# Kernel tuning notes

Measured on AMD Instinct MI355X. Metric: run time of the kernel, lower is better.

The kernel has to match this reference:

```python
import jax, jax.numpy as jnp
import numpy as np

B, S, D_MODEL = 2, 2048, 2048
N_HEADS, N_KV_HEADS, D_HEAD = 32, 8, 64
INIT_STD = 0.02


def setup_inputs() -> dict:
    key = jax.random.key(0)
    k1, k2, k3, k4, k5 = jax.random.split(key, 5)
    return {
        "residual": jax.random.normal(k1, (B, S, D_MODEL), dtype=jnp.float32),
        "W_Q": jax.random.normal(k2, (N_HEADS, D_HEAD, D_MODEL), dtype=jnp.float32) * INIT_STD,
        "W_K": jax.random.normal(k3, (N_KV_HEADS, D_HEAD, D_MODEL), dtype=jnp.float32) * INIT_STD,
        "W_V": jax.random.normal(k4, (N_KV_HEADS, D_HEAD, D_MODEL), dtype=jnp.float32) * INIT_STD,
        "W_O": jax.random.normal(k5, (N_HEADS, D_HEAD, D_MODEL), dtype=jnp.float32) * INIT_STD,
    }


def reference(residual, W_Q, W_K, W_V, W_O):
    # QKV projections: residual [b,p,d] x W [n,h,d] -> [b,p,n,h]
    q = jnp.einsum('bpd,nhd->bpnh', residual, W_Q)
    k = jnp.einsum('bpd,nhd->bpnh', residual, W_K)
    v = jnp.einsum('bpd,nhd->bpnh', residual, W_V)

    # GQA: repeat_interleave kv heads up to n_heads
    rep = N_HEADS // N_KV_HEADS
    k = jnp.repeat(k, rep, axis=2)  # [b, p, n_heads, h]
    v = jnp.repeat(v, rep, axis=2)

    # scaled dot-product scores: [b, n, q, k]
    scores = jnp.einsum('bqnh,bknh->bnqk', q, k) / jnp.sqrt(jnp.float32(D_HEAD))

    # causal mask (seq_len == total_len, no cache)
    seq_len = residual.shape[1]
    causal = jnp.tril(jnp.ones((seq_len, seq_len), dtype=bool))
    scores = jnp.where(causal[None, None, :, :], scores, jnp.float32(-jnp.inf))

    pattern = jax.nn.softmax(scores, axis=-1)

    # weighted sum of values: [b, q, n, h]
    attn_out = jnp.einsum('bnqk,bknh->bqnh', pattern, v)

    # output projection: [b, q, d_model]
    out = jnp.einsum('bqnh,nhd->bqd', attn_out, W_O)
    return out
```

## Files before the change

### kernel.cpp

```cpp
#include <hip/hip_runtime.h>


typedef __attribute__((ext_vector_type(8))) short short8;
typedef __attribute__((ext_vector_type(4))) short short4v;
typedef __attribute__((ext_vector_type(4))) float f32x4;

__device__ __forceinline__ short f2bs(float f) {
  unsigned u = __float_as_uint(f);
  u = (u + 0x7fffu + ((u >> 16) & 1u)) >> 16;
  return (short)u;
}
__device__ __forceinline__ float bs2f(short s) {
  return __uint_as_float(((unsigned)(unsigned short)s) << 16);
}

__device__ __forceinline__ void async_ld16(const void* g, void* l) {
  __builtin_amdgcn_global_load_lds((__attribute__((address_space(1))) void*)(g),
                                   (__attribute__((address_space(3))) void*)(l),
                                   16, 0, 0);
}

#define BARRIER()                       \
  do {                                  \
    asm volatile("" ::: "memory");      \
    __builtin_amdgcn_s_barrier();       \
    asm volatile("" ::: "memory");      \
  } while (0)
#define LGKM0()                                          \
  do {                                                   \
    asm volatile("s_waitcnt lgkmcnt(0)" ::: "memory");   \
    __builtin_amdgcn_sched_barrier(0);                   \
  } while (0)
#define VMCNT(n) asm volatile("s_waitcnt vmcnt(" #n ")" ::: "memory")
#define MFMA16(a, b, c) \
  (c) = __builtin_amdgcn_mfma_f32_16x16x32_bf16((a), (b), (c), 0, 0, 0)

__device__ __forceinline__ short4v pk4bf16(float p0, float p1, float p2,
                                           float p3) {
  union {
    unsigned u[2];
    short4v s;
  } pk;
  asm("v_cvt_pk_bf16_f32 %0, %1, %2" : "=v"(pk.u[0]) : "v"(p0), "v"(p1));
  asm("v_cvt_pk_bf16_f32 %0, %1, %2" : "=v"(pk.u[1]) : "v"(p2), "v"(p3));
  return pk.s;
}

__device__ __forceinline__ int block_sniff_f32(const short* __restrict__ r,
                                               int* bad) {
  if (threadIdx.x == 0) *bad = 0;
  __syncthreads();
  int my = 0;
  for (int i = threadIdx.x; i < 512; i += blockDim.x) {
    float x = bs2f(r[i]);
    if (!(fabsf(x) < 100.0f)) my = 1;
  }
  if (my) atomicOr(bad, 1);
  __syncthreads();
  return *bad;
}

__global__ __launch_bounds__(256) void prep_kernel(
    const void* __restrict__ s0, const void* __restrict__ s1,
    const void* __restrict__ s2, const void* __restrict__ s3,
    short* __restrict__ d0, short* __restrict__ d1, short* __restrict__ d2,
    short* __restrict__ d3, const void* __restrict__ wo,
    short* __restrict__ wot) {
  __shared__ short tile[64][65];
  __shared__ int badsh;
  const int isf = block_sniff_f32((const short*)s0, &badsh);
  const int bid = blockIdx.x;
  if (bid < 7168) {
    long off = (long)bid * 256 + threadIdx.x;
    const void* src;
    short* dst;
    if (off < 1048576) {
      src = s0; dst = d0;
    } else if ((off -= 1048576) < 524288) {
      src = s1; dst = d1;
    } else if ((off -= 524288) < 131072) {
      src = s2; dst = d2;
    } else {
      off -= 131072; src = s3; dst = d3;
    }
    const long e = off * 8;
    short8 v;
    if (isf) {
      const float* f = (const float*)src + e;
      const f32x4 a = *(const f32x4*)(f);
      const f32x4 b = *(const f32x4*)(f + 4);
#pragma unroll
      for (int j = 0; j < 4; ++j) {
        v[j] = f2bs(a[j]);
        v[4 + j] = f2bs(b[j]);
      }
    } else {
      v = *(const short8*)((const short*)src + e);
    }
    *(short8*)(dst + e) = v;
  } else {
    const int tb = bid - 7168;
    const int bx = tb & 31, by = tb >> 5;
    const int tx = threadIdx.x & 63, ty = threadIdx.x >> 6;
#pragma unroll
    for (int i = 0; i < 16; ++i) {
      const int r = ty + i * 4;
      const size_t idx = (size_t)(by * 64 + r) * 2048 + bx * 64 + tx;
      tile[r][tx] =
          isf ? f2bs(((const float*)wo)[idx]) : ((const short*)wo)[idx];
    }
    __syncthreads();
#pragma unroll
    for (int i = 0; i < 16; ++i) {
      const int r = ty + i * 4;
      wot[(size_t)(bx * 64 + r) * 2048 + by * 64 + tx] = tile[tx][r];
    }
  }
}

__device__ __forceinline__ void gemm256(const short* __restrict__ A, int lda,
                                        const short* __restrict__ B, int ldb,
                                        void* __restrict__ C, int ldc,
                                        int rowBase, int colBase, int K,
                                        short* SM, int outF32, int outT,
                                        float cscale) {
  const int t = threadIdx.x;
  const int wave = t >> 6;
  const int lane = t & 63;
  const int quad = lane >> 4;
  const int m16 = lane & 15;
  const int wr = (wave >> 2) * 128;
  const int wc = (wave & 3) * 64;

  short* const As0 = SM;
  short* const As1 = SM + 16384;
  short* const Bs0 = SM + 32768;
  short* const Bs1 = SM + 49152;

  const int sr = t >> 3;
  const int sc8 = ((t & 7) ^ (sr & 7)) * 8;
  const short* aS = A + (size_t)(rowBase + sr) * lda + sc8;
  const short* bS = B + (size_t)(colBase + sr) * ldb + sc8;
  const int dOff = wave * 512;

#define STG_A(buf, rg, kt) \
  async_ld16(aS + (size_t)(rg) * lda + (kt) * 64, (buf) + (rg) * 64 + dOff)
#define STG_B(buf, rg, kt) \
  async_ld16(bS + (size_t)(rg) * ldb + (kt) * 64, (buf) + (rg) * 64 + dOff)
#define RD(buf, row0, kh)                          \
  (*(const short8*)((buf) + ((row0) + m16) * 64 +  \
                    ((((kh) * 4 + quad) ^ (m16 & 7)) * 8)))

  const int nT = K >> 6;
  STG_A(As0, 0, 0); STG_A(As0, 64, 0); STG_A(As0, 128, 0); STG_A(As0, 192, 0);
  STG_B(Bs0, 0, 0); STG_B(Bs0, 64, 0); STG_B(Bs0, 128, 0); STG_B(Bs0, 192, 0);
  if (nT > 1) {
    STG_A(As1, 0, 1); STG_A(As1, 64, 1); STG_A(As1, 128, 1); STG_A(As1, 192, 1);
  }

  f32x4 acc[8][4] = {};
  for (int tt = 0; tt < nT; ++tt) {
    short* const Ac = (tt & 1) ? As1 : As0;
    short* const Bc = (tt & 1) ? Bs1 : Bs0;
    short* const Bn = (tt & 1) ? Bs0 : Bs1;

    if (tt + 1 < nT) {
      VMCNT(4);
    } else {
      VMCNT(0);
    }
    BARRIER();

    if (tt + 1 < nT) {
      STG_B(Bn, 0, tt + 1); STG_B(Bn, 64, tt + 1);
      STG_B(Bn, 128, tt + 1); STG_B(Bn, 192, tt + 1);
    }

    short8 alo[4][2], blo[2][2], bhi[2][2];
#pragma unroll
    for (int i = 0; i < 4; ++i) {
      alo[i][0] = RD(Ac, wr + i * 16, 0);
      alo[i][1] = RD(Ac, wr + i * 16, 1);
    }
#pragma unroll
    for (int j = 0; j < 2; ++j) {
      blo[j][0] = RD(Bc, wc + j * 16, 0);
      blo[j][1] = RD(Bc, wc + j * 16, 1);
    }
#pragma unroll
    for (int i = 0; i < 4; ++i)
#pragma unroll
      for (int j = 0; j < 2; ++j) {
        MFMA16(alo[i][0], blo[j][0], acc[i][j]);
        MFMA16(alo[i][1], blo[j][1], acc[i][j]);
      }
#pragma unroll
    for (int j = 0; j < 2; ++j) {
      bhi[j][0] = RD(Bc, wc + 32 + j * 16, 0);
      bhi[j][1] = RD(Bc, wc + 32 + j * 16, 1);
    }
#pragma unroll
    for (int i = 0; i < 4; ++i)
#pragma unroll
      for (int j = 0; j < 2; ++j) {
        MFMA16(alo[i][0], bhi[j][0], acc[i][2 + j]);
        MFMA16(alo[i][1], bhi[j][1], acc[i][2 + j]);
      }

    short8 ahi[4][2];
#pragma unroll
    for (int i = 0; i < 4; ++i) {
      ahi[i][0] = RD(Ac, wr + 64 + i * 16, 0);
      ahi[i][1] = RD(Ac, wr + 64 + i * 16, 1);
    }
    LGKM0();
    BARRIER();

    if (tt + 2 < nT) {
      STG_A(Ac, 0, tt + 2); STG_A(Ac, 64, tt + 2);
      STG_A(Ac, 128, tt + 2); STG_A(Ac, 192, tt + 2);
    }

#pragma unroll
    for (int i = 0; i < 4; ++i)
#pragma unroll
      for (int j = 0; j < 2; ++j) {
        MFMA16(ahi[i][0], blo[j][0], acc[4 + i][j]);
        MFMA16(ahi[i][1], blo[j][1], acc[4 + i][j]);
      }
#pragma unroll
    for (int i = 0; i < 4; ++i)
#pragma unroll
      for (int j = 0; j < 2; ++j) {
        MFMA16(ahi[i][0], bhi[j][0], acc[4 + i][2 + j]);
        MFMA16(ahi[i][1], bhi[j][1], acc[4 + i][2 + j]);
      }
  }

  float* const F = (float*)SM + wave * 4096;
#pragma unroll
  for (int h = 0; h < 2; ++h) {
    if (h) LGKM0();
#pragma unroll
    for (int i = 0; i < 4; ++i)
#pragma unroll
      for (int j = 0; j < 4; ++j)
#pragma unroll
        for (int r = 0; r < 4; ++r)
          F[(i * 16 + quad * 4 + r) * 64 + j * 16 + m16] =
              acc[h * 4 + i][j][r] * cscale;
    LGKM0();
    if (outT) {
      const int bb = rowBase >> 11;
      const int pBase = (rowBase & 2047) + wr + h * 64;
#pragma unroll
      for (int p2 = 0; p2 < 16; ++p2) {
        const int hl = p2 * 4 + quad;
        short4v s;
#pragma unroll
        for (int r = 0; r < 4; ++r) s[r] = f2bs(F[(m16 * 4 + r) * 64 + hl]);
        *(short4v*)((short*)C +
                    ((size_t)(bb * 512 + colBase + wc + hl)) * ldc + pBase +
                    m16 * 4) = s;
      }
    } else {
#pragma unroll
      for (int p = 0; p < 16; ++p) {
        const int row = p * 4 + quad;
        const f32x4 vv = *(const f32x4*)(F + row * 64 + m16 * 4);
        const size_t gi = (size_t)(rowBase + wr + h * 64 + row) * ldc +
                          colBase + wc + m16 * 4;
        if (outF32) {
          *(f32x4*)((float*)C + gi) = vv;
        } else {
          short4v s;
#pragma unroll
          for (int r = 0; r < 4; ++r) s[r] = f2bs(vv[r]);
          *(short4v*)((short*)C + gi) = s;
        }
      }
    }
  }
#undef STG_A
#undef STG_B
#undef RD
}

__device__ __forceinline__ void gemm256x128(const short* __restrict__ A,
                                            int lda,
                                            const short* __restrict__ B,
                                            int ldb, void* __restrict__ C,
                                            int ldc, int rowBase, int colBase,
                                            int K, short* SM, int outF32) {
  const int t = threadIdx.x;
  const int wave = t >> 6;
  const int lane = t & 63;
  const int quad = lane >> 4;
  const int m16 = lane & 15;
  const int wr = (wave >> 1) * 64;
  const int wc = (wave & 1) * 64;

  short* const As0 = SM;
  short* const As1 = SM + 16384;
  short* const Bs0 = SM + 32768;
  short* const Bs1 = SM + 40960;

  const int sr = t >> 3;
  const int sc8 = ((t & 7) ^ (sr & 7)) * 8;
  const short* aS = A + (size_t)(rowBase + sr) * lda + sc8;
  const short* bS = B + (size_t)(colBase + sr) * ldb + sc8;
  const int dOff = wave * 512;

#define STG_A(buf, rg, kt) \
  async_ld16(aS + (size_t)(rg) * lda + (kt) * 64, (buf) + (rg) * 64 + dOff)
#define STG_B(buf, rg, kt) \
  async_ld16(bS + (size_t)(rg) * ldb + (kt) * 64, (buf) + (rg) * 64 + dOff)
#define RD(buf, row0, kh)                          \
  (*(const short8*)((buf) + ((row0) + m16) * 64 +  \
                    ((((kh) * 4 + quad) ^ (m16 & 7)) * 8)))

  const int nT = K >> 6;
  STG_A(As0, 0, 0); STG_A(As0, 64, 0); STG_A(As0, 128, 0); STG_A(As0, 192, 0);
  STG_B(Bs0, 0, 0); STG_B(Bs0, 64, 0);
  if (nT > 1) {
    STG_A(As1, 0, 1); STG_A(As1, 64, 1); STG_A(As1, 128, 1); STG_A(As1, 192, 1);
  }

  f32x4 acc[4][4] = {};
  for (int tt = 0; tt < nT; ++tt) {
    short* const Ac = (tt & 1) ? As1 : As0;
    short* const Bc = (tt & 1) ? Bs1 : Bs0;
    short* const Bn = (tt & 1) ? Bs0 : Bs1;

    if (tt + 1 < nT) {
      VMCNT(4);
    } else {
      VMCNT(0);
    }
    BARRIER();

    if (tt + 1 < nT) { STG_B(Bn, 0, tt + 1); STG_B(Bn, 64, tt + 1); }

    short8 a0[4], b0[4];
#pragma unroll
    for (int i = 0; i < 4; ++i) a0[i] = RD(Ac, wr + i * 16, 0);
#pragma unroll
    for (int j = 0; j < 4; ++j) b0[j] = RD(Bc, wc + j * 16, 0);
#pragma unroll
    for (int i = 0; i < 4; ++i)
#pragma unroll
      for (int j = 0; j < 4; ++j) MFMA16(a0[i], b0[j], acc[i][j]);

    short8 a1[4], b1[4];
#pragma unroll
    for (int i = 0; i < 4; ++i) a1[i] = RD(Ac, wr + i * 16, 1);
#pragma unroll
    for (int j = 0; j < 4; ++j) b1[j] = RD(Bc, wc + j * 16, 1);
    LGKM0();
    BARRIER();

    if (tt + 2 < nT) {
      STG_A(Ac, 0, tt + 2); STG_A(Ac, 64, tt + 2);
      STG_A(Ac, 128, tt + 2); STG_A(Ac, 192, tt + 2);
    }

#pragma unroll
    for (int i = 0; i < 4; ++i)
#pragma unroll
      for (int j = 0; j < 4; ++j) MFMA16(a1[i], b1[j], acc[i][j]);
  }

  float* const F = (float*)SM + wave * 4096;
#pragma unroll
  for (int i = 0; i < 4; ++i)
#pragma unroll
    for (int j = 0; j < 4; ++j)
#pragma unroll
      for (int r = 0; r < 4; ++r)
        F[(i * 16 + quad * 4 + r) * 64 + j * 16 + m16] = acc[i][j][r];
  LGKM0();
#pragma unroll
  for (int p = 0; p < 16; ++p) {
    const int row = p * 4 + quad;
    const f32x4 vv = *(const f32x4*)(F + row * 64 + m16 * 4);
    const size_t gi =
        (size_t)(rowBase + wr + row) * ldc + colBase + wc + m16 * 4;
    if (outF32) {
      *(f32x4*)((float*)C + gi) = vv;
    } else {
      short4v s;
#pragma unroll
      for (int r = 0; r < 4; ++r) s[r] = f2bs(vv[r]);
      *(short4v*)((short*)C + gi) = s;
    }
  }
#undef STG_A
#undef STG_B
#undef RD
}

__global__ __launch_bounds__(512, 2) void qkv_gemm_kernel(
    const short* __restrict__ R, const short* __restrict__ WQ,
    const short* __restrict__ WK, const short* __restrict__ WV,
    short* __restrict__ q, short* __restrict__ k, short* __restrict__ vtb) {
  __shared__ __align__(16) short SM[65536];
  const int lid = blockIdx.x;
  const int nl = (lid & 7) * 24 + (lid >> 3);
  const int ct = nl % 12;
  const int rt = nl / 12;
  const short* Bm;
  short* Cout;
  int colBase, ldc, outT = 0;
  float cs = 1.0f;
  if (ct < 8) {
    Bm = WQ; Cout = q; colBase = ct * 256; ldc = 2048;
    cs = 0.125f * 1.44269504088896340736f;
  } else if (ct < 10) {
    Bm = WK; Cout = k; colBase = (ct - 8) * 256; ldc = 512;
  } else {
    Bm = WV; Cout = vtb; colBase = (ct - 10) * 256; ldc = 2048; outT = 1;
  }
  gemm256(R, 2048, Bm, 2048, Cout, ldc, rt * 256, colBase, 2048, SM, 0, outT,
          cs);
}

__global__ __launch_bounds__(512, 2) void out_gemm_kernel(
    const short* __restrict__ A, const short* __restrict__ Bt,
    void* __restrict__ C, const short* __restrict__ sniffsrc) {
  __shared__ __align__(16) short SM[65536];
  const int outF32 = block_sniff_f32(sniffsrc, (int*)SM);
  const int lid = blockIdx.x;
  const int nl = (lid & 7) * 32 + (lid >> 3);
  const int ct = nl & 15;
  const int rt = nl >> 4;
  gemm256x128(A, 2048, Bt, 2048, C, 2048, rt * 256, ct * 128, 2048, SM,
              outF32);
}

__global__ __launch_bounds__(256, 3) void attn_kernel(
    const short* __restrict__ qbuf, const short* __restrict__ kbuf,
    const short* __restrict__ vtb, short* __restrict__ obuf) {
  __shared__ __align__(16) short Ks[2][64 * 64];
  __shared__ __align__(16) short Vs[2][64 * 64];
  __shared__ __align__(16) short Pb[4][32 * 64];

  const int b = blockIdx.x >> 3;
  const int kv = blockIdx.x & 7;
  const int qc = 63 - blockIdx.y;
  const int t = threadIdx.x;
  const int wave = t >> 6;
  const int hd = kv * 4 + wave;
  const int lane = t & 63;
  const int quad = lane >> 4;
  const int col = lane & 15;
  const int rb0 = qc * 32;

  short8 qf[2][2];
#pragma unroll
  for (int nt = 0; nt < 2; ++nt) {
    const int qr = rb0 + nt * 16 + col;
    const short* qp = qbuf + ((size_t)(b * 2048 + qr)) * 2048 + hd * 64 + quad * 8;
    qf[nt][0] = *(const short8*)(qp);
    qf[nt][1] = *(const short8*)(qp + 32);
  }

  short8 ones;
#pragma unroll
  for (int i = 0; i < 8; ++i) ones[i] = (short)0x3F80;

  f32x4 oacc[2][4] = {};
  f32x4 sacc[2] = {};

  short* P = &Pb[wave][0];
  const int swz = 4 * (col & 3);

  const int sRow = t >> 3;
  const int sPos = t & 7;
  const int r1 = sRow + 32;
  const short* kRow0 = kbuf + ((size_t)(b * 2048 + sRow)) * 512 + kv * 64 +
                       ((sPos ^ (sRow & 7)) * 8);
  const short* kRow1 = kbuf + ((size_t)(b * 2048 + r1)) * 512 + kv * 64 +
                       ((sPos ^ (r1 & 7)) * 8);
  const short* vRow0 = vtb + ((size_t)(b * 512 + kv * 64 + sRow)) * 2048 +
                       ((sPos ^ (sRow & 7)) * 8);
  const short* vRow1 = vtb + ((size_t)(b * 512 + kv * 64 + r1)) * 2048 +
                       ((sPos ^ (r1 & 7)) * 8);

  const int nkt = (qc >> 1) + 1;

  async_ld16(kRow0, &Ks[0][wave * 512]);
  async_ld16(kRow1, &Ks[0][2048 + wave * 512]);
  async_ld16(vRow0, &Vs[0][wave * 512]);
  async_ld16(vRow1, &Vs[0][2048 + wave * 512]);

  for (int kt = 0; kt < nkt; ++kt) {
    __syncthreads();
    if (kt + 1 < nkt) {
      const int nb = (kt + 1) & 1;
      const size_t ko = (size_t)(kt + 1) * 64 * 512;
      const int vo = (kt + 1) * 64;
      async_ld16(kRow0 + ko, &Ks[nb][wave * 512]);
      async_ld16(kRow1 + ko, &Ks[nb][2048 + wave * 512]);
      async_ld16(vRow0 + vo, &Vs[nb][wave * 512]);
      async_ld16(vRow1 + vo, &Vs[nb][2048 + wave * 512]);
    }
    const int ktb = kt * 64;
    const short* ks = &Ks[kt & 1][0];
    const short* vs = &Vs[kt & 1][0];

    short8 kf[4][2];
#pragma unroll
    for (int mt = 0; mt < 4; ++mt) {
      const int krow = mt * 16 + col;
      kf[mt][0] = *(const short8*)(ks + krow * 64 + ((quad ^ (col & 7)) * 8));
      kf[mt][1] = *(const short8*)(ks + krow * 64 + (((4 + quad) ^ (col & 7)) * 8));
    }

#pragma unroll
    for (int nt = 0; nt < 2; ++nt) {
      const int rb = rb0 + nt * 16;

      f32x4 st[4];
      __builtin_amdgcn_s_setprio(1);
#pragma unroll
      for (int mt = 0; mt < 4; ++mt) {
        f32x4 z = {0.f, 0.f, 0.f, 0.f};
        z = __builtin_amdgcn_mfma_f32_16x16x32_bf16(kf[mt][0], qf[nt][0], z, 0, 0, 0);
        z = __builtin_amdgcn_mfma_f32_16x16x32_bf16(kf[mt][1], qf[nt][1], z, 0, 0, 0);
        st[mt] = z;
      }
      __builtin_amdgcn_s_setprio(0);

      if (ktb + 63 > rb) {
        const int qrow = rb + col;
#pragma unroll
        for (int mt = 0; mt < 4; ++mt)
#pragma unroll
          for (int r = 0; r < 4; ++r)
            if (ktb + mt * 16 + quad * 4 + r > qrow) st[mt][r] = -1.0e30f;
      }

#pragma unroll
      for (int mt = 0; mt < 4; ++mt) {
        const float p0 = exp2f(st[mt][0]);
        const float p1 = exp2f(st[mt][1]);
        const float p2 = exp2f(st[mt][2]);
        const float p3 = exp2f(st[mt][3]);
        *(short4v*)(P + (nt * 16 + col) * 64 + (quad + 4 * (mt ^ (col & 3))) * 4) =
            pk4bf16(p0, p1, p2, p3);
      }
    }

    asm volatile("s_waitcnt lgkmcnt(0)" ::: "memory");

    short8 pf[2][2];
#pragma unroll
    for (int nt = 0; nt < 2; ++nt) {
      const int base = (nt * 16 + col) * 64;
      pf[nt][0] = *(const short8*)(P + base + ((2 * quad) ^ swz) * 4);
      pf[nt][1] = *(const short8*)(P + base + ((8 + 2 * quad) ^ swz) * 4);
    }

    __builtin_amdgcn_s_setprio(1);
#pragma unroll
    for (int nt = 0; nt < 2; ++nt) {
      sacc[nt] = __builtin_amdgcn_mfma_f32_16x16x32_bf16(ones, pf[nt][0],
                                                         sacc[nt], 0, 0, 0);
      sacc[nt] = __builtin_amdgcn_mfma_f32_16x16x32_bf16(ones, pf[nt][1],
                                                         sacc[nt], 0, 0, 0);
    }

#pragma unroll
    for (int ct = 0; ct < 4; ++ct) {
      const int h = ct * 16 + col;
      const short8 va = *(const short8*)(vs + h * 64 + ((quad ^ (col & 7)) * 8));
      const short8 vb = *(const short8*)(vs + h * 64 + (((4 + quad) ^ (col & 7)) * 8));
#pragma unroll
      for (int nt = 0; nt < 2; ++nt) {
        oacc[nt][ct] = __builtin_amdgcn_mfma_f32_16x16x32_bf16(
            va, pf[nt][0], oacc[nt][ct], 0, 0, 0);
        oacc[nt][ct] = __builtin_amdgcn_mfma_f32_16x16x32_bf16(
            vb, pf[nt][1], oacc[nt][ct], 0, 0, 0);
      }
    }
    __builtin_amdgcn_s_setprio(0);
  }

  const float inv0 = 1.0f / sacc[0][0];
  const float inv1 = 1.0f / sacc[1][0];
#pragma unroll
  for (int nt = 0; nt < 2; ++nt) {
    const float inv = nt ? inv1 : inv0;
#pragma unroll
    for (int ct = 0; ct < 4; ++ct) {
      *(short4v*)(P + (nt * 16 + col) * 64 + ct * 16 + quad * 4) =
          pk4bf16(oacc[nt][ct][0] * inv, oacc[nt][ct][1] * inv,
                  oacc[nt][ct][2] * inv, oacc[nt][ct][3] * inv);
    }
  }
  asm volatile("s_waitcnt lgkmcnt(0)" ::: "memory");
#pragma unroll
  for (int p = 0; p < 4; ++p) {
    const int qlocal = (lane >> 3) + 8 * p;
    const short8 row = *(const short8*)(P + qlocal * 64 + (lane & 7) * 8);
    *(short8*)(obuf + ((size_t)(b * 2048 + rb0 + qlocal)) * 2048 + hd * 64 +
               (lane & 7) * 8) = row;
  }
}

extern "C" void kernel_launch(void* const* d_in, const int* in_sizes, int n_in,
                              void* d_out, int out_size, void* d_ws,
                              size_t ws_size, hipStream_t stream) {
  char* ws = (char*)d_ws;
  short* rbuf = (short*)(ws + 256);
  short* wqb = rbuf + 8388608;
  short* wkb = wqb + 4194304;
  short* wvb = wkb + 1048576;
  short* kbuf = wvb + 1048576;
  short* vtb = kbuf + 2097152;
  short* abuf = vtb + 2097152;
  short* wot = abuf + 8388608;
  short* qbuf = (short*)d_out;

  hipLaunchKernelGGL(prep_kernel, dim3(8192), dim3(256), 0, stream,
                     d_in[0], d_in[1], d_in[2], d_in[3], rbuf, wqb, wkb, wvb,
                     d_in[4], wot);
  hipLaunchKernelGGL(qkv_gemm_kernel, dim3(192), dim3(512), 0, stream,
                     rbuf, wqb, wkb, wvb, qbuf, kbuf, vtb);
  hipLaunchKernelGGL(attn_kernel, dim3(16, 64), dim3(256), 0, stream,
                     qbuf, kbuf, vtb, abuf);
  hipLaunchKernelGGL(out_gemm_kernel, dim3(256), dim3(512), 0, stream,
                     abuf, wot, (void*)d_out, (const short*)d_in[0]);
}
```

Before: 289.9 us.

## Switch QKV GEMM to 256x128 tiles, double-buffer B, drop attention setprio

Removes the 256x256 GEMM path and runs the QKV projection on the 256x128 tile routine, extended with output scaling and a transposed-output mode. This doubles the grid from 192 to 384 blocks to fill more CUs. The 256x128 routine now prefetches B two tiles ahead, like A, instead of one. The s_setprio hints around the MFMA blocks in the attention kernel are removed. The smaller tiles mean more operand traffic per FLOP.

```diff
diff --git a/kernel.cpp b/kernel.cpp
--- a/kernel.cpp
+++ b/kernel.cpp
@@ -118,24 +118,25 @@
   }
 }
 
-__device__ __forceinline__ void gemm256(const short* __restrict__ A, int lda,
-                                        const short* __restrict__ B, int ldb,
-                                        void* __restrict__ C, int ldc,
-                                        int rowBase, int colBase, int K,
-                                        short* SM, int outF32, int outT,
-                                        float cscale) {
+__device__ __forceinline__ void gemm256x128(const short* __restrict__ A,
+                                            int lda,
+                                            const short* __restrict__ B,
+                                            int ldb, void* __restrict__ C,
+                                            int ldc, int rowBase, int colBase,
+                                            int K, short* SM, int outF32,
+                                            int outT, float cscale) {
   const int t = threadIdx.x;
   const int wave = t >> 6;
   const int lane = t & 63;
   const int quad = lane >> 4;
   const int m16 = lane & 15;
-  const int wr = (wave >> 2) * 128;
-  const int wc = (wave & 3) * 64;
+  const int wr = (wave >> 1) * 64;
+  const int wc = (wave & 1) * 64;
 
   short* const As0 = SM;
   short* const As1 = SM + 16384;
   short* const Bs0 = SM + 32768;
-  short* const Bs1 = SM + 49152;
+  short* const Bs1 = SM + 40960;
 
   const int sr = t >> 3;
   const int sc8 = ((t & 7) ^ (sr & 7)) * 8;
@@ -153,193 +154,23 @@
 
   const int nT = K >> 6;
   STG_A(As0, 0, 0); STG_A(As0, 64, 0); STG_A(As0, 128, 0); STG_A(As0, 192, 0);
-  STG_B(Bs0, 0, 0); STG_B(Bs0, 64, 0); STG_B(Bs0, 128, 0); STG_B(Bs0, 192, 0);
-  if (nT > 1) {
-    STG_A(As1, 0, 1); STG_A(As1, 64, 1); STG_A(As1, 128, 1); STG_A(As1, 192, 1);
-  }
-
-  f32x4 acc[8][4] = {};
-  for (int tt = 0; tt < nT; ++tt) {
-    short* const Ac = (tt & 1) ? As1 : As0;
-    short* const Bc = (tt & 1) ? Bs1 : Bs0;
-    short* const Bn = (tt & 1) ? Bs0 : Bs1;
-
-    if (tt + 1 < nT) {
-      VMCNT(4);
-    } else {
-      VMCNT(0);
-    }
-    BARRIER();
-
-    if (tt + 1 < nT) {
-      STG_B(Bn, 0, tt + 1); STG_B(Bn, 64, tt + 1);
-      STG_B(Bn, 128, tt + 1); STG_B(Bn, 192, tt + 1);
-    }
-
-    short8 alo[4][2], blo[2][2], bhi[2][2];
-#pragma unroll
-    for (int i = 0; i < 4; ++i) {
-      alo[i][0] = RD(Ac, wr + i * 16, 0);
-      alo[i][1] = RD(Ac, wr + i * 16, 1);
-    }
-#pragma unroll
-    for (int j = 0; j < 2; ++j) {
-      blo[j][0] = RD(Bc, wc + j * 16, 0);
-      blo[j][1] = RD(Bc, wc + j * 16, 1);
-    }
-#pragma unroll
-    for (int i = 0; i < 4; ++i)
-#pragma unroll
-      for (int j = 0; j < 2; ++j) {
-        MFMA16(alo[i][0], blo[j][0], acc[i][j]);
-        MFMA16(alo[i][1], blo[j][1], acc[i][j]);
-      }
-#pragma unroll
-    for (int j = 0; j < 2; ++j) {
-      bhi[j][0] = RD(Bc, wc + 32 + j * 16, 0);
-      bhi[j][1] = RD(Bc, wc + 32 + j * 16, 1);
-    }
-#pragma unroll
-    for (int i = 0; i < 4; ++i)
-#pragma unroll
-      for (int j = 0; j < 2; ++j) {
-        MFMA16(alo[i][0], bhi[j][0], acc[i][2 + j]);
-        MFMA16(alo[i][1], bhi[j][1], acc[i][2 + j]);
-      }
-
-    short8 ahi[4][2];
-#pragma unroll
-    for (int i = 0; i < 4; ++i) {
-      ahi[i][0] = RD(Ac, wr + 64 + i * 16, 0);
-      ahi[i][1] = RD(Ac, wr + 64 + i * 16, 1);
-    }
-    LGKM0();
-    BARRIER();
-
-    if (tt + 2 < nT) {
-      STG_A(Ac, 0, tt + 2); STG_A(Ac, 64, tt + 2);
-      STG_A(Ac, 128, tt + 2); STG_A(Ac, 192, tt + 2);
-    }
-
-#pragma unroll
-    for (int i = 0; i < 4; ++i)
-#pragma unroll
-      for (int j = 0; j < 2; ++j) {
-        MFMA16(ahi[i][0], blo[j][0], acc[4 + i][j]);
-        MFMA16(ahi[i][1], blo[j][1], acc[4 + i][j]);
-      }
-#pragma unroll
-    for (int i = 0; i < 4; ++i)
-#pragma unroll
-      for (int j = 0; j < 2; ++j) {
-        MFMA16(ahi[i][0], bhi[j][0], acc[4 + i][2 + j]);
-        MFMA16(ahi[i][1], bhi[j][1], acc[4 + i][2 + j]);
-      }
-  }
-
-  float* const F = (float*)SM + wave * 4096;
-#pragma unroll
-  for (int h = 0; h < 2; ++h) {
-    if (h) LGKM0();
-#pragma unroll
-    for (int i = 0; i < 4; ++i)
-#pragma unroll
-      for (int j = 0; j < 4; ++j)
-#pragma unroll
-        for (int r = 0; r < 4; ++r)
-          F[(i * 16 + quad * 4 + r) * 64 + j * 16 + m16] =
-              acc[h * 4 + i][j][r] * cscale;
-    LGKM0();
-    if (outT) {
-      const int bb = rowBase >> 11;
-      const int pBase = (rowBase & 2047) + wr + h * 64;
-#pragma unroll
-      for (int p2 = 0; p2 < 16; ++p2) {
-        const int hl = p2 * 4 + quad;
-        short4v s;
-#pragma unroll
-        for (int r = 0; r < 4; ++r) s[r] = f2bs(F[(m16 * 4 + r) * 64 + hl]);
-        *(short4v*)((short*)C +
-                    ((size_t)(bb * 512 + colBase + wc + hl)) * ldc + pBase +
-                    m16 * 4) = s;
-      }
-    } else {
-#pragma unroll
-      for (int p = 0; p < 16; ++p) {
-        const int row = p * 4 + quad;
-        const f32x4 vv = *(const f32x4*)(F + row * 64 + m16 * 4);
-        const size_t gi = (size_t)(rowBase + wr + h * 64 + row) * ldc +
-                          colBase + wc + m16 * 4;
-        if (outF32) {
-          *(f32x4*)((float*)C + gi) = vv;
-        } else {
-          short4v s;
-#pragma unroll
-          for (int r = 0; r < 4; ++r) s[r] = f2bs(vv[r]);
-          *(short4v*)((short*)C + gi) = s;
-        }
-      }
-    }
-  }
-#undef STG_A
-#undef STG_B
-#undef RD
-}
-
-__device__ __forceinline__ void gemm256x128(const short* __restrict__ A,
-                                            int lda,
-                                            const short* __restrict__ B,
-                                            int ldb, void* __restrict__ C,
-                                            int ldc, int rowBase, int colBase,
-                                            int K, short* SM, int outF32) {
-  const int t = threadIdx.x;
-  const int wave = t >> 6;
-  const int lane = t & 63;
-  const int quad = lane >> 4;
-  const int m16 = lane & 15;
-  const int wr = (wave >> 1) * 64;
-  const int wc = (wave & 1) * 64;
-
-  short* const As0 = SM;
-  short* const As1 = SM + 16384;
-  short* const Bs0 = SM + 32768;
-  short* const Bs1 = SM + 40960;
-
-  const int sr = t >> 3;
-  const int sc8 = ((t & 7) ^ (sr & 7)) * 8;
-  const short* aS = A + (size_t)(rowBase + sr) * lda + sc8;
-  const short* bS = B + (size_t)(colBase + sr) * ldb + sc8;
-  const int dOff = wave * 512;
-
-#define STG_A(buf, rg, kt) \
-  async_ld16(aS + (size_t)(rg) * lda + (kt) * 64, (buf) + (rg) * 64 + dOff)
-#define STG_B(buf, rg, kt) \
-  async_ld16(bS + (size_t)(rg) * ldb + (kt) * 64, (buf) + (rg) * 64 + dOff)
-#define RD(buf, row0, kh)                          \
-  (*(const short8*)((buf) + ((row0) + m16) * 64 +  \
-                    ((((kh) * 4 + quad) ^ (m16 & 7)) * 8)))
-
-  const int nT = K >> 6;
-  STG_A(As0, 0, 0); STG_A(As0, 64, 0); STG_A(As0, 128, 0); STG_A(As0, 192, 0);
   STG_B(Bs0, 0, 0); STG_B(Bs0, 64, 0);
   if (nT > 1) {
     STG_A(As1, 0, 1); STG_A(As1, 64, 1); STG_A(As1, 128, 1); STG_A(As1, 192, 1);
+    STG_B(Bs1, 0, 1); STG_B(Bs1, 64, 1);
   }
 
   f32x4 acc[4][4] = {};
   for (int tt = 0; tt < nT; ++tt) {
     short* const Ac = (tt & 1) ? As1 : As0;
     short* const Bc = (tt & 1) ? Bs1 : Bs0;
-    short* const Bn = (tt & 1) ? Bs0 : Bs1;
 
     if (tt + 1 < nT) {
-      VMCNT(4);
+      VMCNT(6);
     } else {
       VMCNT(0);
     }
     BARRIER();
-
-    if (tt + 1 < nT) { STG_B(Bn, 0, tt + 1); STG_B(Bn, 64, tt + 1); }
 
     short8 a0[4], b0[4];
 #pragma unroll
@@ -362,6 +193,7 @@
     if (tt + 2 < nT) {
       STG_A(Ac, 0, tt + 2); STG_A(Ac, 64, tt + 2);
       STG_A(Ac, 128, tt + 2); STG_A(Ac, 192, tt + 2);
+      STG_B(Bc, 0, tt + 2); STG_B(Bc, 64, tt + 2);
     }
 
 #pragma unroll
@@ -377,21 +209,36 @@
     for (int j = 0; j < 4; ++j)
 #pragma unroll
       for (int r = 0; r < 4; ++r)
-        F[(i * 16 + quad * 4 + r) * 64 + j * 16 + m16] = acc[i][j][r];
+        F[(i * 16 + quad * 4 + r) * 64 + j * 16 + m16] =
+            acc[i][j][r] * cscale;
   LGKM0();
-#pragma unroll
-  for (int p = 0; p < 16; ++p) {
-    const int row = p * 4 + quad;
-    const f32x4 vv = *(const f32x4*)(F + row * 64 + m16 * 4);
-    const size_t gi =
-        (size_t)(rowBase + wr + row) * ldc + colBase + wc + m16 * 4;
-    if (outF32) {
-      *(f32x4*)((float*)C + gi) = vv;
-    } else {
+  if (outT) {
+    const int bb = rowBase >> 11;
+    const int pBase = (rowBase & 2047) + wr;
+#pragma unroll
+    for (int p2 = 0; p2 < 16; ++p2) {
+      const int hl = p2 * 4 + quad;
       short4v s;
 #pragma unroll
-      for (int r = 0; r < 4; ++r) s[r] = f2bs(vv[r]);
-      *(short4v*)((short*)C + gi) = s;
+      for (int r = 0; r < 4; ++r) s[r] = f2bs(F[(m16 * 4 + r) * 64 + hl]);
+      *(short4v*)((short*)C + ((size_t)(bb * 512 + colBase + wc + hl)) * ldc +
+                  pBase + m16 * 4) = s;
+    }
+  } else {
+#pragma unroll
+    for (int p = 0; p < 16; ++p) {
+      const int row = p * 4 + quad;
+      const f32x4 vv = *(const f32x4*)(F + row * 64 + m16 * 4);
+      const size_t gi =
+          (size_t)(rowBase + wr + row) * ldc + colBase + wc + m16 * 4;
+      if (outF32) {
+        *(f32x4*)((float*)C + gi) = vv;
+      } else {
+        short4v s;
+#pragma unroll
+        for (int r = 0; r < 4; ++r) s[r] = f2bs(vv[r]);
+        *(short4v*)((short*)C + gi) = s;
+      }
     }
   }
 #undef STG_A
@@ -405,23 +252,23 @@
     short* __restrict__ q, short* __restrict__ k, short* __restrict__ vtb) {
   __shared__ __align__(16) short SM[65536];
   const int lid = blockIdx.x;
-  const int nl = (lid & 7) * 24 + (lid >> 3);
-  const int ct = nl % 12;
-  const int rt = nl / 12;
+  const int nl = (lid & 7) * 48 + (lid >> 3);
+  const int ct = nl % 24;
+  const int rt = nl / 24;
   const short* Bm;
   short* Cout;
   int colBase, ldc, outT = 0;
   float cs = 1.0f;
-  if (ct < 8) {
-    Bm = WQ; Cout = q; colBase = ct * 256; ldc = 2048;
+  if (ct < 16) {
+    Bm = WQ; Cout = q; colBase = ct * 128; ldc = 2048;
     cs = 0.125f * 1.44269504088896340736f;
-  } else if (ct < 10) {
-    Bm = WK; Cout = k; colBase = (ct - 8) * 256; ldc = 512;
+  } else if (ct < 20) {
+    Bm = WK; Cout = k; colBase = (ct - 16) * 128; ldc = 512;
   } else {
-    Bm = WV; Cout = vtb; colBase = (ct - 10) * 256; ldc = 2048; outT = 1;
-  }
-  gemm256(R, 2048, Bm, 2048, Cout, ldc, rt * 256, colBase, 2048, SM, 0, outT,
-          cs);
+    Bm = WV; Cout = vtb; colBase = (ct - 20) * 128; ldc = 2048; outT = 1;
+  }
+  gemm256x128(R, 2048, Bm, 2048, Cout, ldc, rt * 256, colBase, 2048, SM, 0,
+              outT, cs);
 }
 
 __global__ __launch_bounds__(512, 2) void out_gemm_kernel(
@@ -434,7 +281,7 @@
   const int ct = nl & 15;
   const int rt = nl >> 4;
   gemm256x128(A, 2048, Bt, 2048, C, 2048, rt * 256, ct * 128, 2048, SM,
-              outF32);
+              outF32, 0, 1.0f);
 }
 
 __global__ __launch_bounds__(256, 3) void attn_kernel(
@@ -521,7 +368,6 @@
       const int rb = rb0 + nt * 16;
 
       f32x4 st[4];
-      __builtin_amdgcn_s_setprio(1);
 #pragma unroll
       for (int mt = 0; mt < 4; ++mt) {
         f32x4 z = {0.f, 0.f, 0.f, 0.f};
@@ -529,7 +375,6 @@
         z = __builtin_amdgcn_mfma_f32_16x16x32_bf16(kf[mt][1], qf[nt][1], z, 0, 0, 0);
         st[mt] = z;
       }
-      __builtin_amdgcn_s_setprio(0);
 
       if (ktb + 63 > rb) {
         const int qrow = rb + col;
@@ -561,7 +406,6 @@
       pf[nt][1] = *(const short8*)(P + base + ((8 + 2 * quad) ^ swz) * 4);
     }
 
-    __builtin_amdgcn_s_setprio(1);
 #pragma unroll
     for (int nt = 0; nt < 2; ++nt) {
       sacc[nt] = __builtin_amdgcn_mfma_f32_16x16x32_bf16(ones, pf[nt][0],
@@ -583,7 +427,6 @@
             vb, pf[nt][1], oacc[nt][ct], 0, 0, 0);
       }
     }
-    __builtin_amdgcn_s_setprio(0);
   }
 
   const float inv0 = 1.0f / sacc[0][0];
@@ -625,7 +468,7 @@
   hipLaunchKernelGGL(prep_kernel, dim3(8192), dim3(256), 0, stream,
                      d_in[0], d_in[1], d_in[2], d_in[3], rbuf, wqb, wkb, wvb,
                      d_in[4], wot);
-  hipLaunchKernelGGL(qkv_gemm_kernel, dim3(192), dim3(512), 0, stream,
+  hipLaunchKernelGGL(qkv_gemm_kernel, dim3(384), dim3(512), 0, stream,
                      rbuf, wqb, wkb, wvb, qbuf, kbuf, vtb);
   hipLaunchKernelGGL(attn_kernel, dim3(16, 64), dim3(256), 0, stream,
                      qbuf, kbuf, vtb, abuf);
```

Measured after the change: 289.3 us. About the same (-0.2%).
